# Performance work log

Hardware: AMD Instinct MI355X
Metric: run time of the kernel (lower is better)

The kernel has to match this reference:

```python
import jax, jax.numpy as jnp
import numpy as np

N = 20000      # tuple-graph nodes
E = 320000     # edges per relation
F_IN = 5189    # 80 one-hot + 3*1703 node features
DIM = 256
N_ORIG = 183   # original texas graph nodes
C = 7


def _gcn(x, W, b, src, dst, n):
    # PyG GCNConv: add self loops, symmetric deg^-1/2 normalization, aggregate src->dst.
    loop = jnp.arange(n)
    s = jnp.concatenate([src, loop])
    d = jnp.concatenate([dst, loop])
    deg = jax.ops.segment_sum(jnp.ones(s.shape[0], x.dtype), d, num_segments=n)
    dinv = jnp.where(deg > 0, jax.lax.rsqrt(deg), 0.0)
    norm = dinv[s] * dinv[d]            # [E+n]
    h = x @ W                            # [n, dim]
    out = jax.ops.segment_sum(h[s] * norm[:, None], d, num_segments=n)
    return out + b


def _mlp(h, w1, b1, w2, b2):
    return jnp.maximum(h @ w1 + b1, 0.0) @ w2 + b2


def _seg_mean(h, idx, n):
    s = jax.ops.segment_sum(h, idx, num_segments=n)
    cnt = jax.ops.segment_sum(jnp.ones(idx.shape[0], h.dtype), idx, num_segments=n)
    return s / jnp.maximum(cnt, 1.0)[:, None]


def setup_inputs() -> dict:
    key = jax.random.key(0)
    ks = jax.random.split(key, 16)
    sc_in = 1.0 / np.sqrt(F_IN)
    sc_d = 1.0 / np.sqrt(DIM)
    sc_3d = 1.0 / np.sqrt(3 * DIM)
    inp = {
        'x': jax.random.normal(ks[0], (N, F_IN), jnp.float32),
        'w1': jax.random.normal(ks[1], (3, F_IN, DIM), jnp.float32) * sc_in,
        'b1': jnp.zeros((3, DIM), jnp.float32),
        'w2': jax.random.normal(ks[2], (3, DIM, DIM), jnp.float32) * sc_d,
        'b2': jnp.zeros((3, DIM), jnp.float32),
        'm1w1': jax.random.normal(ks[3], (3 * DIM, DIM), jnp.float32) * sc_3d,
        'm1b1': jnp.zeros((DIM,), jnp.float32),
        'm1w2': jax.random.normal(ks[4], (DIM, DIM), jnp.float32) * sc_d,
        'm1b2': jnp.zeros((DIM,), jnp.float32),
        'm2w1': jax.random.normal(ks[5], (3 * DIM, DIM), jnp.float32) * sc_3d,
        'm2b1': jnp.zeros((DIM,), jnp.float32),
        'm2w2': jax.random.normal(ks[6], (DIM, DIM), jnp.float32) * sc_d,
        'm2b2': jnp.zeros((DIM,), jnp.float32),
        'mw1': jax.random.normal(ks[7], (3 * DIM, DIM), jnp.float32) * sc_3d,
        'mb1': jnp.zeros((DIM,), jnp.float32),
        'mw2': jax.random.normal(ks[8], (DIM, C), jnp.float32) * sc_d,
        'mb2': jnp.zeros((C,), jnp.float32),
        'edge_index_1': jax.random.randint(ks[9], (2, E), 0, N),
        'edge_index_2': jax.random.randint(ks[10], (2, E), 0, N),
        'edge_index_3': jax.random.randint(ks[11], (2, E), 0, N),
        'index_1': jax.random.randint(ks[12], (N,), 0, N_ORIG),
        'index_2': jax.random.randint(ks[13], (N,), 0, N_ORIG),
        'index_3': jax.random.randint(ks[14], (N,), 0, N_ORIG),
    }
    return inp


def reference(x, w1, b1, w2, b2, m1w1, m1b1, m1w2, m1b2,
              m2w1, m2b1, m2w2, m2b2, mw1, mb1, mw2, mb2,
              edge_index_1, edge_index_2, edge_index_3,
              index_1, index_2, index_3):
    n = x.shape[0]
    eis = (edge_index_1, edge_index_2, edge_index_3)
    # layer 1: three GCN convs over the three relations, ReLU, concat, MLP
    hs = [jnp.maximum(_gcn(x, w1[i], b1[i], eis[i][0], eis[i][1], n), 0.0) for i in range(3)]
    h = _mlp(jnp.concatenate(hs, axis=-1), m1w1, m1b1, m1w2, m1b2)
    # layer 2
    hs = [jnp.maximum(_gcn(h, w2[i], b2[i], eis[i][0], eis[i][1], n), 0.0) for i in range(3)]
    h = _mlp(jnp.concatenate(hs, axis=-1), m2w1, m2b1, m2w2, m2b2)
    # faithful to source bug: index_2 is overwritten by index_3 before scatter
    x1 = _seg_mean(h, index_1, N_ORIG)
    x2 = _seg_mean(h, index_3, N_ORIG)
    x3 = _seg_mean(h, index_3, N_ORIG)
    out = _mlp(jnp.concatenate([x1, x2, x3], axis=1), mw1, mb1, mw2, mb2)
    return jax.nn.log_softmax(out, axis=1)
```

## Files before the change

### kernel.cpp

```cpp
#include <hip/hip_runtime.h>
#include <hip/hip_bf16.h>
#include <cstdint>
#include <cstddef>

typedef __bf16 bf16_t;
typedef __bf16 bf16x8 __attribute__((ext_vector_type(8)));
typedef __bf16 bf16x4 __attribute__((ext_vector_type(4)));
typedef float f32x4 __attribute__((ext_vector_type(4)));

#define NN 20000
#define NE 320000
#define FIN 5189
#define KP1 5216
#define NORIG 183

__device__ inline f32x4 ld4u(const float* p) {
  f32x4 v; __builtin_memcpy(&v, p, 16); return v;
}

__device__ inline void gload_lds16(const bf16_t* g, bf16_t* l) {
  __builtin_amdgcn_global_load_lds(
      (const __attribute__((address_space(1))) uint32_t*)g,
      (__attribute__((address_space(3))) uint32_t*)l, 16, 0, 0);
}

__device__ inline int swz(int r) { return (r ^ (r >> 2)) & 3; }

__global__ void k_cvtpad(const float* __restrict__ x, bf16_t* __restrict__ xb) {
  const int total = NN * (KP1 / 8);
  for (int idx = blockIdx.x * 256 + threadIdx.x; idx < total; idx += gridDim.x * 256) {
    int row = idx / (KP1 / 8);
    int c8  = idx - row * (KP1 / 8);
    int col = c8 * 8;
    bf16x8 v{};
    const float* xp = x + (size_t)row * FIN + col;
    if (col + 8 <= FIN) {
      f32x4 a = ld4u(xp), b = ld4u(xp + 4);
#pragma unroll
      for (int j = 0; j < 4; ++j) { v[j] = (bf16_t)a[j]; v[4 + j] = (bf16_t)b[j]; }
    } else {
#pragma unroll
      for (int j = 0; j < 8; ++j) v[j] = (col + j < FIN) ? (bf16_t)xp[j] : (bf16_t)0.f;
    }
    *(bf16x8*)&xb[(size_t)row * KP1 + col] = v;
  }
}

__global__ __launch_bounds__(512) void k_gemm_w(
    const bf16_t* __restrict__ A, const bf16_t* __restrict__ Bt,
    bf16_t* __restrict__ C, const float* __restrict__ bias,
    const float* __restrict__ dscale,
    int M, int N, int Kp, int relu, int NBX)
{
  __shared__ __align__(16) bf16_t As[2][128 * 32];
  __shared__ __align__(16) bf16_t Bs[2][256 * 32];
  const int nwg = gridDim.x;
  const int q = nwg >> 3, rr = nwg & 7;
  const int xcd = blockIdx.x & 7, jj = blockIdx.x >> 3;
  const int L = (xcd < rr ? xcd * (q + 1) : rr * (q + 1) + (xcd - rr) * q) + jj;
  const int bx = L % NBX, by = L / NBX;

  const int tid = threadIdx.x, lane = tid & 63, wave = tid >> 6;
  const int m0 = by * 128, n0 = bx * 256;
  const int wr = (wave >> 2) * 64, wc = (wave & 3) * 64;
  const int fm = lane & 15, fs = lane >> 4;

  const int arow = tid >> 2, asl = tid & 3;
  const int aks = asl ^ swz(arow);
  int agrow = m0 + arow; if (agrow >= M) agrow = M - 1;
  const bf16_t* asrc = A + (size_t)agrow * Kp + aks * 8;

  const int br0 = tid >> 2, br1 = 128 + br0;
  const bf16_t* bsrc0 = Bt + (size_t)(n0 + br0) * Kp + (asl ^ swz(br0)) * 8;
  const bf16_t* bsrc1 = Bt + (size_t)(n0 + br1) * Kp + (asl ^ swz(br1)) * 8;

  bf16_t* adst  = &As[0][0] + wave * 512;
  bf16_t* bdst0 = &Bs[0][0] + wave * 512;
  bf16_t* bdst1 = &Bs[0][0] + 4096 + wave * 512;

  int aoff[4], boff[4];
#pragma unroll
  for (int i = 0; i < 4; ++i) {
    int ra = wr + i * 16 + fm;
    aoff[i] = ra * 32 + (fs ^ swz(ra)) * 8;
    int rb = wc + i * 16 + fm;
    boff[i] = rb * 32 + (fs ^ swz(rb)) * 8;
  }

  f32x4 acc[4][4];
#pragma unroll
  for (int i = 0; i < 4; ++i)
#pragma unroll
    for (int j = 0; j < 4; ++j) acc[i][j] = {0.f, 0.f, 0.f, 0.f};

#define STAGEW(buf, kof) do { \
    gload_lds16(asrc + (kof),  adst  + (buf) * (128 * 32)); \
    gload_lds16(bsrc0 + (kof), bdst0 + (buf) * (256 * 32)); \
    gload_lds16(bsrc1 + (kof), bdst1 + (buf) * (256 * 32)); \
  } while (0)

  const int NT = Kp / 32;
  STAGEW(0, 0);
  __syncthreads();
  int buf = 0;
  for (int t = 0; t < NT - 1; ++t) {
    STAGEW(buf ^ 1, (t + 1) * 32);
    bf16x8 af[4], bfv[4];
#pragma unroll
    for (int i = 0; i < 4; ++i) af[i] = *(const bf16x8*)&As[buf][aoff[i]];
#pragma unroll
    for (int j = 0; j < 4; ++j) bfv[j] = *(const bf16x8*)&Bs[buf][boff[j]];
#pragma unroll
    for (int i = 0; i < 4; ++i)
#pragma unroll
      for (int j = 0; j < 4; ++j)
        acc[i][j] = __builtin_amdgcn_mfma_f32_16x16x32_bf16(af[i], bfv[j], acc[i][j], 0, 0, 0);
    __syncthreads();
    buf ^= 1;
  }
  {
    bf16x8 af[4], bfv[4];
#pragma unroll
    for (int i = 0; i < 4; ++i) af[i] = *(const bf16x8*)&As[buf][aoff[i]];
#pragma unroll
    for (int j = 0; j < 4; ++j) bfv[j] = *(const bf16x8*)&Bs[buf][boff[j]];
#pragma unroll
    for (int i = 0; i < 4; ++i)
#pragma unroll
      for (int j = 0; j < 4; ++j)
        acc[i][j] = __builtin_amdgcn_mfma_f32_16x16x32_bf16(af[i], bfv[j], acc[i][j], 0, 0, 0);
  }

  const int ccol = n0 + wc + fm;
  const int rrel = (n0 + wc) >> 8;
  const float* dsp = dscale ? dscale + (size_t)rrel * NN : nullptr;
#pragma unroll
  for (int i = 0; i < 4; ++i) {
    const int rb2 = m0 + wr + i * 16 + (lane >> 4) * 4;
#pragma unroll
    for (int r = 0; r < 4; ++r) {
      const int row = rb2 + r;
      if (row < M) {
        bf16_t* cp = C + (size_t)row * N + ccol;
        const float sc = dsp ? dsp[row] : 1.f;
#pragma unroll
        for (int j = 0; j < 4; ++j) {
          float v = acc[i][j][r];
          if (bias) v += bias[ccol + j * 16];
          if (relu) v = fmaxf(v, 0.f);
          cp[j * 16] = (bf16_t)(v * sc);
        }
      }
    }
  }
}

__global__ __launch_bounds__(256) void k_gemm_s(
    const bf16_t* __restrict__ A, const bf16_t* __restrict__ Bt,
    bf16_t* __restrict__ C, const float* __restrict__ bias,
    int M, int N, int Kp, int relu)
{
  __shared__ __align__(16) bf16_t As[2][128 * 32];
  __shared__ __align__(16) bf16_t Bs[2][128 * 32];
  const int tid = threadIdx.x, lane = tid & 63, wave = tid >> 6;
  const int m0 = blockIdx.y * 128, n0 = blockIdx.x * 128;
  const int wr = (wave >> 1) * 64, wc = (wave & 1) * 64;
  const int fm = lane & 15, fs = lane >> 4;

  const int r0 = tid >> 2, r1 = 64 + r0, sl = tid & 3;
  int ag0 = m0 + r0; if (ag0 >= M) ag0 = M - 1;
  int ag1 = m0 + r1; if (ag1 >= M) ag1 = M - 1;
  const bf16_t* asrc0 = A + (size_t)ag0 * Kp + (sl ^ swz(r0)) * 8;
  const bf16_t* asrc1 = A + (size_t)ag1 * Kp + (sl ^ swz(r1)) * 8;
  const bf16_t* bsrc0 = Bt + (size_t)(n0 + r0) * Kp + (sl ^ swz(r0)) * 8;
  const bf16_t* bsrc1 = Bt + (size_t)(n0 + r1) * Kp + (sl ^ swz(r1)) * 8;

  bf16_t* adst0 = &As[0][0] + wave * 512;
  bf16_t* adst1 = &As[0][0] + 2048 + wave * 512;
  bf16_t* bdst0 = &Bs[0][0] + wave * 512;
  bf16_t* bdst1 = &Bs[0][0] + 2048 + wave * 512;

  int aoff[4], boff[4];
#pragma unroll
  for (int i = 0; i < 4; ++i) {
    int ra = wr + i * 16 + fm;
    aoff[i] = ra * 32 + (fs ^ swz(ra)) * 8;
    int rb = wc + i * 16 + fm;
    boff[i] = rb * 32 + (fs ^ swz(rb)) * 8;
  }

  f32x4 acc[4][4];
#pragma unroll
  for (int i = 0; i < 4; ++i)
#pragma unroll
    for (int j = 0; j < 4; ++j) acc[i][j] = {0.f, 0.f, 0.f, 0.f};

#define STAGES(buf, kof) do { \
    gload_lds16(asrc0 + (kof), adst0 + (buf) * (128 * 32)); \
    gload_lds16(asrc1 + (kof), adst1 + (buf) * (128 * 32)); \
    gload_lds16(bsrc0 + (kof), bdst0 + (buf) * (128 * 32)); \
    gload_lds16(bsrc1 + (kof), bdst1 + (buf) * (128 * 32)); \
  } while (0)

  const int NT = Kp / 32;
  STAGES(0, 0);
  __syncthreads();
  int buf = 0;
  for (int t = 0; t < NT - 1; ++t) {
    STAGES(buf ^ 1, (t + 1) * 32);
    bf16x8 af[4], bfv[4];
#pragma unroll
    for (int i = 0; i < 4; ++i) af[i] = *(const bf16x8*)&As[buf][aoff[i]];
#pragma unroll
    for (int j = 0; j < 4; ++j) bfv[j] = *(const bf16x8*)&Bs[buf][boff[j]];
#pragma unroll
    for (int i = 0; i < 4; ++i)
#pragma unroll
      for (int j = 0; j < 4; ++j)
        acc[i][j] = __builtin_amdgcn_mfma_f32_16x16x32_bf16(af[i], bfv[j], acc[i][j], 0, 0, 0);
    __syncthreads();
    buf ^= 1;
  }
  {
    bf16x8 af[4], bfv[4];
#pragma unroll
    for (int i = 0; i < 4; ++i) af[i] = *(const bf16x8*)&As[buf][aoff[i]];
#pragma unroll
    for (int j = 0; j < 4; ++j) bfv[j] = *(const bf16x8*)&Bs[buf][boff[j]];
#pragma unroll
    for (int i = 0; i < 4; ++i)
#pragma unroll
      for (int j = 0; j < 4; ++j)
        acc[i][j] = __builtin_amdgcn_mfma_f32_16x16x32_bf16(af[i], bfv[j], acc[i][j], 0, 0, 0);
  }

  const int ccol = n0 + wc + fm;
#pragma unroll
  for (int i = 0; i < 4; ++i) {
    const int rb2 = m0 + wr + i * 16 + (lane >> 4) * 4;
#pragma unroll
    for (int r = 0; r < 4; ++r) {
      const int row = rb2 + r;
      if (row < M) {
        bf16_t* cp = C + (size_t)row * N + ccol;
#pragma unroll
        for (int j = 0; j < 4; ++j) {
          float v = acc[i][j][r];
          if (bias) v += bias[ccol + j * 16];
          if (relu) v = fmaxf(v, 0.f);
          cp[j * 16] = (bf16_t)v;
        }
      }
    }
  }
}

__global__ void k_transw(const float* __restrict__ src, bf16_t* __restrict__ dst,
                         int K, int Kp)
{
  __shared__ float tile[32][33];
  const int g = blockIdx.z;
  const int k0 = blockIdx.x * 32, j0 = blockIdx.y * 32;
  const int tx = threadIdx.x, ty = threadIdx.y;
  const float* sp = src + (size_t)g * K * 256;
#pragma unroll
  for (int i = 0; i < 4; ++i) {
    int k = k0 + ty + i * 8;
    tile[ty + i * 8][tx] = (k < K) ? sp[(size_t)k * 256 + j0 + tx] : 0.f;
  }
  __syncthreads();
  bf16_t* dp = dst + (size_t)g * 256 * Kp;
#pragma unroll
  for (int i = 0; i < 4; ++i) {
    int n = j0 + ty + i * 8;
    dp[(size_t)n * Kp + k0 + tx] = (bf16_t)tile[tx][ty + i * 8];
  }
}

__global__ void k_deg3(const int* __restrict__ e1, const int* __restrict__ e2,
                       const int* __restrict__ e3, int* __restrict__ deg) {
  int i = blockIdx.x * 256 + threadIdx.x;
  if (i >= 3 * NE) return;
  int r = i / NE, e = i - r * NE;
  const int* d = (r == 0 ? e1 : (r == 1 ? e2 : e3)) + NE;
  atomicAdd(&deg[r * NN + d[e]], 1);
}

__global__ void k_degi(const int* __restrict__ i1, const int* __restrict__ i3,
                       int* __restrict__ deg183) {
  int i = blockIdx.x * 256 + threadIdx.x;
  if (i >= 2 * NN) return;
  int r = i / NN, v = i - r * NN;
  int g = (r ? i3 : i1)[v];
  atomicAdd(&deg183[r * NORIG + g], 1);
}

__global__ void k_dinv(const int* __restrict__ deg, float* __restrict__ dinv) {
  int v = blockIdx.x * 256 + threadIdx.x;
  if (v < 3 * NN) dinv[v] = rsqrtf((float)(deg[v] + 1));
}

#define SCAN_T 1024
#define SCAN_CH 20
__global__ __launch_bounds__(SCAN_T) void k_scan(
    const int* __restrict__ deg, int* __restrict__ rp, int* __restrict__ cur)
{
  const int r = blockIdx.x;
  const int* d = deg + r * NN;
  int* rpr = rp + r * (NN + 1);
  int* cr  = cur + r * NN;
  __shared__ int ts[SCAN_T];
  const int t = threadIdx.x;
  const int base = t * SCAN_CH;
  int local[SCAN_CH];
  int sum = 0;
#pragma unroll
  for (int i = 0; i < SCAN_CH; ++i) {
    int v = base + i;
    int x = (v < NN) ? d[v] : 0;
    local[i] = sum; sum += x;
  }
  ts[t] = sum; __syncthreads();
  for (int ofs = 1; ofs < SCAN_T; ofs <<= 1) {
    int v = ts[t];
    int w = (t >= ofs) ? ts[t - ofs] : 0;
    __syncthreads();
    ts[t] = v + w;
    __syncthreads();
  }
  int excl = (t == 0) ? 0 : ts[t - 1];
#pragma unroll
  for (int i = 0; i < SCAN_CH; ++i) {
    int v = base + i;
    if (v < NN) { int val = excl + local[i]; rpr[v] = val; cr[v] = val; }
  }
  if (t == SCAN_T - 1) rpr[NN] = ts[SCAN_T - 1];
}

__global__ void k_scan183(const int* __restrict__ deg183, int* __restrict__ rpg,
                          int* __restrict__ cur183) {
  const int r = blockIdx.x;
  const int* d = deg183 + r * NORIG;
  int* rpr = rpg + r * (NORIG + 1);
  int* cr  = cur183 + r * NORIG;
  __shared__ int ts[256];
  const int t = threadIdx.x;
  int x = (t < NORIG) ? d[t] : 0;
  ts[t] = x; __syncthreads();
  for (int o = 1; o < 256; o <<= 1) {
    int v = ts[t];
    int w = (t >= o) ? ts[t - o] : 0;
    __syncthreads();
    ts[t] = v + w;
    __syncthreads();
  }
  if (t < NORIG) {
    int excl = ts[t] - x;
    rpr[t] = excl; cr[t] = excl;
    if (t == NORIG - 1) rpr[NORIG] = ts[t];
  }
}

__global__ void k_bucket3(const int* __restrict__ e1, const int* __restrict__ e2,
                          const int* __restrict__ e3, int* __restrict__ cur,
                          int* __restrict__ col) {
  int i = blockIdx.x * 256 + threadIdx.x;
  if (i >= 3 * NE) return;
  int r = i / NE, e = i - r * NE;
  const int* ei = (r == 0 ? e1 : (r == 1 ? e2 : e3));
  int d = ei[NE + e];
  int pos = atomicAdd(&cur[r * NN + d], 1);
  col[(size_t)r * NE + pos] = ei[e];
}

__global__ void k_bucketi(const int* __restrict__ i1, const int* __restrict__ i3,
                          int* __restrict__ cur183, int* __restrict__ colg) {
  int i = blockIdx.x * 256 + threadIdx.x;
  if (i >= 2 * NN) return;
  int r = i / NN, v = i - r * NN;
  int g = (r ? i3 : i1)[v];
  int pos = atomicAdd(&cur183[r * NORIG + g], 1);
  colg[r * NN + pos] = v;
}

__global__ __launch_bounds__(256) void k_gatherb(
    const bf16_t* __restrict__ P, bf16_t* __restrict__ Out,
    const int* __restrict__ rp, const int* __restrict__ col,
    const float* __restrict__ dinv, const float* __restrict__ bias)
{
  const int wv = threadIdx.x >> 6, lane = threadIdx.x & 63;
  const int v = blockIdx.x * 4 + wv;
  const int r = blockIdx.y;
  const int roff = r << 8;
  const int* rpr = rp + r * (NN + 1);
  const int* cr  = col + (size_t)r * NE;
  const float dv = dinv[r * NN + v];
  const int c0 = roff + lane * 4;

  bf16x4 hs = *(const bf16x4*)&P[(size_t)v * 768 + c0];
  float a0 = (float)hs[0], a1 = (float)hs[1], a2 = (float)hs[2], a3 = (float)hs[3];

  int i = rpr[v];
  const int e = rpr[v + 1];
  for (; i + 16 <= e; i += 16) {
    bf16x4 h[16];
#pragma unroll
    for (int u = 0; u < 16; ++u) {
      int s = cr[i + u];
      h[u] = *(const bf16x4*)&P[(size_t)s * 768 + c0];
    }
#pragma unroll
    for (int u = 0; u < 16; ++u) {
      a0 += (float)h[u][0]; a1 += (float)h[u][1];
      a2 += (float)h[u][2]; a3 += (float)h[u][3];
    }
  }
  for (; i + 4 <= e; i += 4) {
    bf16x4 h[4];
#pragma unroll
    for (int u = 0; u < 4; ++u) {
      int s = cr[i + u];
      h[u] = *(const bf16x4*)&P[(size_t)s * 768 + c0];
    }
#pragma unroll
    for (int u = 0; u < 4; ++u) {
      a0 += (float)h[u][0]; a1 += (float)h[u][1];
      a2 += (float)h[u][2]; a3 += (float)h[u][3];
    }
  }
  for (; i < e; ++i) {
    int s = cr[i];
    bf16x4 h = *(const bf16x4*)&P[(size_t)s * 768 + c0];
    a0 += (float)h[0]; a1 += (float)h[1];
    a2 += (float)h[2]; a3 += (float)h[3];
  }
  f32x4 bb = ld4u(bias + c0);
  bf16x4 o;
  o[0] = (bf16_t)fmaxf(dv * a0 + bb[0], 0.f);
  o[1] = (bf16_t)fmaxf(dv * a1 + bb[1], 0.f);
  o[2] = (bf16_t)fmaxf(dv * a2 + bb[2], 0.f);
  o[3] = (bf16_t)fmaxf(dv * a3 + bb[3], 0.f);
  *(bf16x4*)&Out[(size_t)v * 768 + c0] = o;
}

__global__ __launch_bounds__(256) void k_final2(
    const bf16_t* __restrict__ h2,
    const int* __restrict__ rpg, const int* __restrict__ colg,
    const float* __restrict__ mw1, const float* __restrict__ mb1,
    const float* __restrict__ mw2, const float* __restrict__ mb2,
    float* __restrict__ out)
{
  __shared__ float xc[768];
  __shared__ float tt[256];
  __shared__ float lg[8];
  const int g = blockIdx.x, tid = threadIdx.x;
  const int* rp1 = rpg;
  const int* rp3 = rpg + (NORIG + 1);
  const int* c1v = colg;
  const int* c3v = colg + NN;

  float a1 = 0.f;
  int b1 = rp1[g], e1 = rp1[g + 1];
  for (int i = b1; i < e1; ++i) a1 += (float)h2[(size_t)c1v[i] * 256 + tid];
  float a3 = 0.f;
  int b3 = rp3[g], e3 = rp3[g + 1];
  for (int i = b3; i < e3; ++i) a3 += (float)h2[(size_t)c3v[i] * 256 + tid];
  a1 *= 1.f / fmaxf((float)(e1 - b1), 1.f);
  a3 *= 1.f / fmaxf((float)(e3 - b3), 1.f);
  xc[tid] = a1;
  xc[256 + tid] = a3;
  xc[512 + tid] = a3;
  __syncthreads();
  float acc = mb1[tid];
  for (int k = 0; k < 768; ++k) acc += xc[k] * mw1[k * 256 + tid];
  tt[tid] = fmaxf(acc, 0.f);
  __syncthreads();
  if (tid < 7) {
    float a = mb2[tid];
    for (int k = 0; k < 256; ++k) a += tt[k] * mw2[k * 7 + tid];
    lg[tid] = a;
  }
  __syncthreads();
  if (tid == 0) {
    float mx = lg[0];
    for (int c2 = 1; c2 < 7; ++c2) mx = fmaxf(mx, lg[c2]);
    float sum = 0.f;
    for (int c2 = 0; c2 < 7; ++c2) sum += expf(lg[c2] - mx);
    float lse = logf(sum) + mx;
    for (int c2 = 0; c2 < 7; ++c2) out[g * 7 + c2] = lg[c2] - lse;
  }
}

extern "C" void kernel_launch(void* const* d_in, const int* in_sizes, int n_in,
                              void* d_out, int out_size, void* d_ws, size_t ws_size,
                              hipStream_t stream) {
  const float* x    = (const float*)d_in[0];
  const float* w1   = (const float*)d_in[1];
  const float* b1   = (const float*)d_in[2];
  const float* w2   = (const float*)d_in[3];
  const float* b2   = (const float*)d_in[4];
  const float* m1w1 = (const float*)d_in[5];
  const float* m1b1 = (const float*)d_in[6];
  const float* m1w2 = (const float*)d_in[7];
  const float* m1b2 = (const float*)d_in[8];
  const float* m2w1 = (const float*)d_in[9];
  const float* m2b1 = (const float*)d_in[10];
  const float* m2w2 = (const float*)d_in[11];
  const float* m2b2 = (const float*)d_in[12];
  const float* mw1  = (const float*)d_in[13];
  const float* mb1  = (const float*)d_in[14];
  const float* mw2  = (const float*)d_in[15];
  const float* mb2  = (const float*)d_in[16];
  const int* e1 = (const int*)d_in[17];
  const int* e2 = (const int*)d_in[18];
  const int* e3 = (const int*)d_in[19];
  const int* i1 = (const int*)d_in[20];
  const int* i3 = (const int*)d_in[22];
  float* out = (float*)d_out;

  char* ws = (char*)d_ws;
  size_t off = 0;
  auto alloc = [&](size_t bytes) {
    char* p = ws + off;
    off += (bytes + 255) & ~(size_t)255;
    return (void*)p;
  };
  bf16_t* xb   = (bf16_t*)alloc((size_t)NN * KP1 * 2);
  bf16_t* wt   = (bf16_t*)alloc((size_t)768 * KP1 * 2);
  bf16_t* a1   = (bf16_t*)alloc((size_t)NN * 768 * 2);
  bf16_t* g1   = (bf16_t*)alloc((size_t)NN * 768 * 2);
  bf16_t* t1   = (bf16_t*)alloc((size_t)NN * 256 * 2);
  bf16_t* h1   = (bf16_t*)alloc((size_t)NN * 256 * 2);
  int*    deg  = (int*)alloc(((size_t)3 * NN + 2 * NORIG) * 4);
  float*  dinv = (float*)alloc((size_t)3 * NN * 4);
  int*    rp   = (int*)alloc((size_t)3 * (NN + 1) * 4);
  int*    cur  = (int*)alloc((size_t)3 * NN * 4);
  int*    col  = (int*)alloc((size_t)3 * NE * 4);
  int*    rpg  = (int*)alloc((size_t)2 * (NORIG + 1) * 4);
  int*    cur183 = (int*)alloc((size_t)2 * NORIG * 4);
  int*    colg = (int*)alloc((size_t)2 * NN * 4);
  int*    deg183 = deg + 3 * NN;

  hipMemsetAsync(deg, 0, ((size_t)3 * NN + 2 * NORIG) * 4, stream);
  k_deg3<<<(3 * NE + 255) / 256, 256, 0, stream>>>(e1, e2, e3, deg);
  k_degi<<<(2 * NN + 255) / 256, 256, 0, stream>>>(i1, i3, deg183);
  k_dinv<<<(3 * NN + 255) / 256, 256, 0, stream>>>(deg, dinv);
  k_scan<<<3, SCAN_T, 0, stream>>>(deg, rp, cur);
  k_scan183<<<2, 256, 0, stream>>>(deg183, rpg, cur183);
  k_bucket3<<<(3 * NE + 255) / 256, 256, 0, stream>>>(e1, e2, e3, cur, col);
  k_bucketi<<<(2 * NN + 255) / 256, 256, 0, stream>>>(i1, i3, cur183, colg);

  auto transw = [&](const float* Wsrc, int G, int K, int Kp) {
    k_transw<<<dim3(Kp / 32, 8, G), dim3(32, 8), 0, stream>>>(Wsrc, wt, K, Kp);
  };

  dim3 ggat(NN / 4, 3);
  const int NWGW = 3 * 157;

  transw(w1, 3, FIN, KP1);
  k_cvtpad<<<2048, 256, 0, stream>>>(x, xb);
  k_gemm_w<<<NWGW, 512, 0, stream>>>(xb, wt, a1, nullptr, dinv, NN, 768, KP1, 0, 3);
  k_gatherb<<<ggat, 256, 0, stream>>>(a1, g1, rp, col, dinv, b1);
  transw(m1w1, 1, 768, 768);
  k_gemm_s<<<dim3(2, 157), 256, 0, stream>>>(g1, wt, t1, m1b1, NN, 256, 768, 1);
  transw(m1w2, 1, 256, 256);
  k_gemm_s<<<dim3(2, 157), 256, 0, stream>>>(t1, wt, h1, m1b2, NN, 256, 256, 0);

  transw(w2, 3, 256, 256);
  k_gemm_w<<<NWGW, 512, 0, stream>>>(h1, wt, a1, nullptr, dinv, NN, 768, 256, 0, 3);
  k_gatherb<<<ggat, 256, 0, stream>>>(a1, g1, rp, col, dinv, b2);
  transw(m2w1, 1, 768, 768);
  k_gemm_s<<<dim3(2, 157), 256, 0, stream>>>(g1, wt, t1, m2b1, NN, 256, 768, 1);
  transw(m2w2, 1, 256, 256);
  k_gemm_s<<<dim3(2, 157), 256, 0, stream>>>(t1, wt, h1, m2b2, NN, 256, 256, 0);

  k_final2<<<NORIG, 256, 0, stream>>>(h1, rpg, colg, mw1, mb1, mw2, mb2, out);
}
```

Before: 885.4 us.

## Triple-buffer GEMM LDS staging with partial vmcnt waits

Replaces the double-buffered K loop in k_gemm_w with a three-stage ring buffer. Two tiles are prefetched ahead, and each iteration waits only until the older load group has landed (vmcnt(3)) before the barrier, so global-to-LDS traffic overlaps more MFMA work. This raises shared memory use by half, which may reduce occupancy, and relies on hand-written waitcnt and sched_barrier ordering being correct.

```diff
diff --git a/kernel.cpp b/kernel.cpp
--- a/kernel.cpp
+++ b/kernel.cpp
@@ -52,8 +52,8 @@
     const float* __restrict__ dscale,
     int M, int N, int Kp, int relu, int NBX)
 {
-  __shared__ __align__(16) bf16_t As[2][128 * 32];
-  __shared__ __align__(16) bf16_t Bs[2][256 * 32];
+  __shared__ __align__(16) bf16_t As[3][128 * 32];
+  __shared__ __align__(16) bf16_t Bs[3][256 * 32];
   const int nwg = gridDim.x;
   const int q = nwg >> 3, rr = nwg & 7;
   const int xcd = blockIdx.x & 7, jj = blockIdx.x >> 3;
@@ -101,35 +101,36 @@
 
   const int NT = Kp / 32;
   STAGEW(0, 0);
-  __syncthreads();
-  int buf = 0;
-  for (int t = 0; t < NT - 1; ++t) {
-    STAGEW(buf ^ 1, (t + 1) * 32);
+  STAGEW(1, 32);
+  __builtin_amdgcn_sched_barrier(0);
+  asm volatile("s_waitcnt vmcnt(3)" ::: "memory");
+  __builtin_amdgcn_s_barrier();
+  __builtin_amdgcn_sched_barrier(0);
+
+  int cb = 0, sb = 2;
+  for (int u = 0; u < NT; ++u) {
+    if (u + 2 < NT) STAGEW(sb, (u + 2) * 32);
     bf16x8 af[4], bfv[4];
 #pragma unroll
-    for (int i = 0; i < 4; ++i) af[i] = *(const bf16x8*)&As[buf][aoff[i]];
-#pragma unroll
-    for (int j = 0; j < 4; ++j) bfv[j] = *(const bf16x8*)&Bs[buf][boff[j]];
+    for (int i = 0; i < 4; ++i) af[i] = *(const bf16x8*)&As[cb][aoff[i]];
+#pragma unroll
+    for (int j = 0; j < 4; ++j) bfv[j] = *(const bf16x8*)&Bs[cb][boff[j]];
 #pragma unroll
     for (int i = 0; i < 4; ++i)
 #pragma unroll
       for (int j = 0; j < 4; ++j)
         acc[i][j] = __builtin_amdgcn_mfma_f32_16x16x32_bf16(af[i], bfv[j], acc[i][j], 0, 0, 0);
-    __syncthreads();
-    buf ^= 1;
-  }
-  {
-    bf16x8 af[4], bfv[4];
-#pragma unroll
-    for (int i = 0; i < 4; ++i) af[i] = *(const bf16x8*)&As[buf][aoff[i]];
-#pragma unroll
-    for (int j = 0; j < 4; ++j) bfv[j] = *(const bf16x8*)&Bs[buf][boff[j]];
-#pragma unroll
-    for (int i = 0; i < 4; ++i)
-#pragma unroll
-      for (int j = 0; j < 4; ++j)
-        acc[i][j] = __builtin_amdgcn_mfma_f32_16x16x32_bf16(af[i], bfv[j], acc[i][j], 0, 0, 0);
-  }
+    if (u + 1 < NT) {
+      __builtin_amdgcn_sched_barrier(0);
+      if (u + 2 < NT) asm volatile("s_waitcnt vmcnt(3) lgkmcnt(0)" ::: "memory");
+      else            asm volatile("s_waitcnt vmcnt(0) lgkmcnt(0)" ::: "memory");
+      __builtin_amdgcn_s_barrier();
+      __builtin_amdgcn_sched_barrier(0);
+    }
+    cb = (cb == 2) ? 0 : cb + 1;
+    sb = (sb == 2) ? 0 : sb + 1;
+  }
+#undef STAGEW
 
   const int ccol = n0 + wc + fm;
   const int rrel = (n0 + wc) >> 8;
```

Result: no change. 881.6 us (-0.4%).
